# Performance work log

Measured on AMD Instinct MI355X. Metric: run time of the kernel, lower is better.

The kernel has to match this reference:

```python
import jax, jax.numpy as jnp
import numpy as np

B, S, D, O = 8, 2048, 1024, 1024  # batch, seq_len, state_dim(=input_dim), output_dim


def setup_inputs() -> dict:
    key = jax.random.key(0)
    k_in, k_a, k_bc = jax.random.split(key, 3)
    inputs = jax.random.normal(k_in, (B, S, D), dtype=jnp.float32)
    # Stable diagonal transition (|A| < 1) so the 2048-step recurrence stays bounded.
    A = jax.random.uniform(k_a, (D,), minval=-0.99, maxval=0.99, dtype=jnp.float32)
    BC = jax.random.normal(k_bc, (D, O), dtype=jnp.float32) / D
    return {"inputs": inputs, "A": A, "BC": BC}


def reference(inputs, A, BC):
    # Diagonal LTI recurrence: h_t = A * h_{t-1} + x_t ; out_t = h_t @ BC
    # h0 = zeros (the module's h0 Parameter is initialized to zeros).
    x_tfirst = jnp.swapaxes(inputs, 0, 1)  # [S, B, D]

    def step(h, x_t):
        h = h * A + x_t
        return h, h

    h0 = jnp.zeros((inputs.shape[0], A.shape[0]), dtype=inputs.dtype)
    _, hs = jax.lax.scan(step, h0, x_tfirst)  # hs: [S, B, D]
    # Single fused projection over all timesteps instead of per-step matmuls.
    out = jnp.einsum('sbd,do->bso', hs, BC)  # [B, S, O]
    return out
```

## Files before the change

kernel.cpp:

```cpp
#include <hip/hip_runtime.h>
#include <hip/hip_bf16.h>

#define BB 8
#define SS 2048
#define DD 1024
#define OO 1024
#define MM (BB * SS)
#define KK DD
#define NN OO
#define CC 32
#define LL 64

typedef __bf16 bf16x8 __attribute__((ext_vector_type(8)));
typedef __bf16 bf16x4 __attribute__((ext_vector_type(4)));
typedef float floatx4 __attribute__((ext_vector_type(4)));

__global__ __launch_bounds__(256) void scan_carry(const float* __restrict__ x,
                                                  const float* __restrict__ A,
                                                  float* __restrict__ carry) {
    const int i4 = threadIdx.x;
    const int c = blockIdx.x;
    const int b = blockIdx.y;
    const float4 a = ((const float4*)A)[i4];
    const float4* xp = (const float4*)(x + ((size_t)b * SS + (size_t)c * LL) * DD) + i4;
    float4 h = make_float4(0.f, 0.f, 0.f, 0.f);
#pragma unroll 8
    for (int t = 0; t < LL; ++t) {
        const float4 v = xp[(size_t)t * (DD / 4)];
        h.x = fmaf(h.x, a.x, v.x);
        h.y = fmaf(h.y, a.y, v.y);
        h.z = fmaf(h.z, a.z, v.z);
        h.w = fmaf(h.w, a.w, v.w);
    }
    ((float4*)carry)[((size_t)b * CC + c) * (DD / 4) + i4] = h;
}

__global__ void chunk_scan(const float* __restrict__ carry, const float* __restrict__ A,
                           float* __restrict__ Hprev) {
    const int idx = blockIdx.x * 256 + threadIdx.x;
    const int d = idx & (DD - 1);
    const int b = idx >> 10;
    const float a = A[d];
    float aL = a;
#pragma unroll
    for (int i = 0; i < 6; ++i) aL *= aL;
    float h = 0.f;
#pragma unroll
    for (int c = 0; c < CC; ++c) {
        const size_t o = ((size_t)b * CC + c) * DD + d;
        Hprev[o] = h;
        h = fmaf(aL, h, carry[o]);
    }
}

__global__ __launch_bounds__(256) void scan_emit(const float* __restrict__ x,
                                                 const float* __restrict__ A,
                                                 const float* __restrict__ Hprev,
                                                 __bf16* __restrict__ hs) {
    const int i4 = threadIdx.x;
    const int c = blockIdx.x;
    const int b = blockIdx.y;
    const float4 a = ((const float4*)A)[i4];
    float4 h = ((const float4*)Hprev)[((size_t)b * CC + c) * (DD / 4) + i4];
    const size_t base = ((size_t)b * SS + (size_t)c * LL) * DD;
    const float4* xp = (const float4*)(x + base) + i4;
    bf16x4* hp = (bf16x4*)(hs + base) + i4;
#pragma unroll 4
    for (int t = 0; t < LL; ++t) {
        const float4 v = xp[(size_t)t * (DD / 4)];
        h.x = fmaf(h.x, a.x, v.x);
        h.y = fmaf(h.y, a.y, v.y);
        h.z = fmaf(h.z, a.z, v.z);
        h.w = fmaf(h.w, a.w, v.w);
        bf16x4 o;
        o[0] = (__bf16)h.x; o[1] = (__bf16)h.y; o[2] = (__bf16)h.z; o[3] = (__bf16)h.w;
        hp[(size_t)t * (DD / 4)] = o;
    }
}

__global__ void transpose_cast(const float* __restrict__ BC, __bf16* __restrict__ BCt) {
    __shared__ float tile[32][33];
    const int tx = threadIdx.x & 31;
    const int ty = threadIdx.x >> 5;
    const int o0 = blockIdx.x * 32;
    const int d0 = blockIdx.y * 32;
#pragma unroll
    for (int i = 0; i < 4; ++i) {
        const int dd = ty + i * 8;
        tile[dd][tx] = BC[(size_t)(d0 + dd) * OO + o0 + tx];
    }
    __syncthreads();
#pragma unroll
    for (int i = 0; i < 4; ++i) {
        const int oo = ty + i * 8;
        BCt[(size_t)(o0 + oo) * DD + d0 + tx] = (__bf16)tile[tx][oo];
    }
}

#define TM 128
#define TN 128
#define TK 32

__device__ __forceinline__ void async16(void* lds, const void* g) {
    __builtin_amdgcn_global_load_lds(
        (__attribute__((address_space(1))) void*)(void*)g,
        (__attribute__((address_space(3))) void*)lds, 16, 0, 0);
}

__global__ __launch_bounds__(256) void gemm_bt(const __bf16* __restrict__ Am,
                                               const __bf16* __restrict__ Bt,
                                               float* __restrict__ C) {
    __shared__ __align__(16) __bf16 As[TM * TK];
    __shared__ __align__(16) __bf16 Bs[TN * TK];

    const int tid = threadIdx.x;
    const int wave = tid >> 6;
    const int lane = tid & 63;
    const int wm = (wave >> 1) * 64;
    const int wn = (wave & 1) * 64;
    const int lanelo = lane & 15;
    const int quad = lane >> 4;
    const int tile_m = blockIdx.x * TM;
    const int tile_n = blockIdx.y * TN;

    const int cid0 = tid;
    const int cid1 = tid + 256;
    const int r0 = cid0 >> 2, q0 = (cid0 & 3) * 8;
    const int r1 = cid1 >> 2, q1 = (cid1 & 3) * 8;

    floatx4 acc[4][4];
#pragma unroll
    for (int i = 0; i < 4; ++i)
#pragma unroll
        for (int j = 0; j < 4; ++j) acc[i][j] = (floatx4){0.f, 0.f, 0.f, 0.f};

    for (int k0 = 0; k0 < KK; k0 += TK) {
        __syncthreads();
        async16(&As[cid0 * 8], Am + (size_t)(tile_m + r0) * KK + k0 + q0);
        async16(&As[cid1 * 8], Am + (size_t)(tile_m + r1) * KK + k0 + q1);
        async16(&Bs[cid0 * 8], Bt + (size_t)(tile_n + r0) * KK + k0 + q0);
        async16(&Bs[cid1 * 8], Bt + (size_t)(tile_n + r1) * KK + k0 + q1);
        __syncthreads();

        bf16x8 af[4], bf[4];
#pragma unroll
        for (int i = 0; i < 4; ++i)
            af[i] = *(const bf16x8*)(&As[(wm + i * 16 + lanelo) * TK + quad * 8]);
#pragma unroll
        for (int j = 0; j < 4; ++j)
            bf[j] = *(const bf16x8*)(&Bs[(wn + j * 16 + lanelo) * TK + quad * 8]);

#pragma unroll
        for (int i = 0; i < 4; ++i)
#pragma unroll
            for (int j = 0; j < 4; ++j)
                acc[i][j] = __builtin_amdgcn_mfma_f32_16x16x32_bf16(af[i], bf[j], acc[i][j], 0, 0, 0);
    }

#pragma unroll
    for (int i = 0; i < 4; ++i) {
        const int row = tile_m + wm + i * 16 + quad * 4;
#pragma unroll
        for (int r = 0; r < 4; ++r) {
            float* crow = C + (size_t)(row + r) * NN + tile_n + wn + lanelo;
#pragma unroll
            for (int j = 0; j < 4; ++j) crow[j * 16] = acc[i][j][r];
        }
    }
}

extern "C" void kernel_launch(void* const* d_in, const int* in_sizes, int n_in,
                              void* d_out, int out_size, void* d_ws, size_t ws_size,
                              hipStream_t stream) {
    const float* x  = (const float*)d_in[0];
    const float* A  = (const float*)d_in[1];
    const float* BC = (const float*)d_in[2];
    float* out = (float*)d_out;

    char* ws = (char*)d_ws;
    __bf16* hs   = (__bf16*)ws;
    float* carry = (float*)(ws + 33554432);
    float* Hprev = (float*)(ws + 33554432 + 1048576);
    __bf16* BCt  = (__bf16*)(ws + 33554432 + 2097152);

    scan_carry<<<dim3(CC, BB), 256, 0, stream>>>(x, A, carry);
    transpose_cast<<<dim3(OO / 32, DD / 32), 256, 0, stream>>>(BC, BCt);
    chunk_scan<<<dim3(BB * DD / 256), 256, 0, stream>>>(carry, A, Hprev);
    scan_emit<<<dim3(CC, BB), 256, 0, stream>>>(x, A, Hprev, hs);
    gemm_bt<<<dim3(MM / TM, NN / TN), 256, 0, stream>>>(hs, BCt, out);
}
```

Measured before the change: 180.4 us.

## Double scan chunk count, fuse carry scan with BC transpose, batch loads

Raises the number of sequence chunks from 32 to 64 (length 32 each), doubling the blocks in the carry and emit scan kernels so more CUs are busy during these memory-bound phases. The carry scan and the BC transpose-cast are merged into one launch, removing a kernel launch. Loads of x are grouped eight at a time to raise memory-level parallelism, and chunk_scan preloads all carries into registers before the serial pass. The trade-off is a longer serial chunk_scan, more carry and Hprev traffic, and higher register use in chunk_scan.

Result: no change. 179.0 us (-0.8%).

```diff
diff --git a/kernel.cpp b/kernel.cpp
--- a/kernel.cpp
+++ b/kernel.cpp
@@ -8,48 +8,83 @@
 #define MM (BB * SS)
 #define KK DD
 #define NN OO
-#define CC 32
-#define LL 64
+#define CC 64
+#define LL 32
 
 typedef __bf16 bf16x8 __attribute__((ext_vector_type(8)));
 typedef __bf16 bf16x4 __attribute__((ext_vector_type(4)));
 typedef float floatx4 __attribute__((ext_vector_type(4)));
 
-__global__ __launch_bounds__(256) void scan_carry(const float* __restrict__ x,
+__device__ __forceinline__ float4 fma4(float4 h, float4 a, float4 v) {
+    h.x = fmaf(h.x, a.x, v.x);
+    h.y = fmaf(h.y, a.y, v.y);
+    h.z = fmaf(h.z, a.z, v.z);
+    h.w = fmaf(h.w, a.w, v.w);
+    return h;
+}
+
+__global__ __launch_bounds__(256) void prep(const float* __restrict__ x,
+                                            const float* __restrict__ A,
+                                            float* __restrict__ carry,
+                                            const float* __restrict__ BC,
+                                            __bf16* __restrict__ BCt) {
+    __shared__ float tile[32][33];
+    const int id = blockIdx.x;
+    if (id < BB * CC) {
+        const int c = id & (CC - 1);
+        const int b = id >> 6;
+        const int i4 = threadIdx.x;
+        const float4 a = ((const float4*)A)[i4];
+        const float4* xp = (const float4*)(x + ((size_t)b * SS + (size_t)c * LL) * DD) + i4;
+        float4 h = make_float4(0.f, 0.f, 0.f, 0.f);
+#pragma unroll
+        for (int t0 = 0; t0 < LL; t0 += 8) {
+            float4 v[8];
+#pragma unroll
+            for (int u = 0; u < 8; ++u) v[u] = xp[(size_t)(t0 + u) * (DD / 4)];
+#pragma unroll
+            for (int u = 0; u < 8; ++u) h = fma4(h, a, v[u]);
+        }
+        ((float4*)carry)[((size_t)b * CC + c) * (DD / 4) + i4] = h;
+    } else {
+        const int t = id - BB * CC;
+        const int o0 = (t & 31) * 32;
+        const int d0 = (t >> 5) * 32;
+        const int tx = threadIdx.x & 31;
+        const int ty = threadIdx.x >> 5;
+#pragma unroll
+        for (int i = 0; i < 4; ++i) {
+            const int dd = ty + i * 8;
+            tile[dd][tx] = BC[(size_t)(d0 + dd) * OO + o0 + tx];
+        }
+        __syncthreads();
+#pragma unroll
+        for (int i = 0; i < 4; ++i) {
+            const int oo = ty + i * 8;
+            BCt[(size_t)(o0 + oo) * DD + d0 + tx] = (__bf16)tile[tx][oo];
+        }
+    }
+}
+
+__global__ __launch_bounds__(256) void chunk_scan(const float* __restrict__ carry,
                                                   const float* __restrict__ A,
-                                                  float* __restrict__ carry) {
-    const int i4 = threadIdx.x;
-    const int c = blockIdx.x;
-    const int b = blockIdx.y;
-    const float4 a = ((const float4*)A)[i4];
-    const float4* xp = (const float4*)(x + ((size_t)b * SS + (size_t)c * LL) * DD) + i4;
-    float4 h = make_float4(0.f, 0.f, 0.f, 0.f);
-#pragma unroll 8
-    for (int t = 0; t < LL; ++t) {
-        const float4 v = xp[(size_t)t * (DD / 4)];
-        h.x = fmaf(h.x, a.x, v.x);
-        h.y = fmaf(h.y, a.y, v.y);
-        h.z = fmaf(h.z, a.z, v.z);
-        h.w = fmaf(h.w, a.w, v.w);
-    }
-    ((float4*)carry)[((size_t)b * CC + c) * (DD / 4) + i4] = h;
-}
-
-__global__ void chunk_scan(const float* __restrict__ carry, const float* __restrict__ A,
-                           float* __restrict__ Hprev) {
+                                                  float* __restrict__ Hprev) {
     const int idx = blockIdx.x * 256 + threadIdx.x;
     const int d = idx & (DD - 1);
     const int b = idx >> 10;
     const float a = A[d];
     float aL = a;
 #pragma unroll
-    for (int i = 0; i < 6; ++i) aL *= aL;
+    for (int i = 0; i < 5; ++i) aL *= aL;
+    float ca[CC];
+#pragma unroll
+    for (int c = 0; c < CC; ++c)
+        ca[c] = carry[((size_t)b * CC + c) * DD + d];
     float h = 0.f;
 #pragma unroll
     for (int c = 0; c < CC; ++c) {
-        const size_t o = ((size_t)b * CC + c) * DD + d;
-        Hprev[o] = h;
-        h = fmaf(aL, h, carry[o]);
+        Hprev[((size_t)b * CC + c) * DD + d] = h;
+        h = fmaf(aL, h, ca[c]);
     }
 }
 
@@ -57,43 +92,27 @@
                                                  const float* __restrict__ A,
                                                  const float* __restrict__ Hprev,
                                                  __bf16* __restrict__ hs) {
+    const int id = blockIdx.x;
+    const int c = id & (CC - 1);
+    const int b = id >> 6;
     const int i4 = threadIdx.x;
-    const int c = blockIdx.x;
-    const int b = blockIdx.y;
     const float4 a = ((const float4*)A)[i4];
     float4 h = ((const float4*)Hprev)[((size_t)b * CC + c) * (DD / 4) + i4];
     const size_t base = ((size_t)b * SS + (size_t)c * LL) * DD;
     const float4* xp = (const float4*)(x + base) + i4;
     bf16x4* hp = (bf16x4*)(hs + base) + i4;
-#pragma unroll 4
-    for (int t = 0; t < LL; ++t) {
-        const float4 v = xp[(size_t)t * (DD / 4)];
-        h.x = fmaf(h.x, a.x, v.x);
-        h.y = fmaf(h.y, a.y, v.y);
-        h.z = fmaf(h.z, a.z, v.z);
-        h.w = fmaf(h.w, a.w, v.w);
-        bf16x4 o;
-        o[0] = (__bf16)h.x; o[1] = (__bf16)h.y; o[2] = (__bf16)h.z; o[3] = (__bf16)h.w;
-        hp[(size_t)t * (DD / 4)] = o;
-    }
-}
-
-__global__ void transpose_cast(const float* __restrict__ BC, __bf16* __restrict__ BCt) {
-    __shared__ float tile[32][33];
-    const int tx = threadIdx.x & 31;
-    const int ty = threadIdx.x >> 5;
-    const int o0 = blockIdx.x * 32;
-    const int d0 = blockIdx.y * 32;
-#pragma unroll
-    for (int i = 0; i < 4; ++i) {
-        const int dd = ty + i * 8;
-        tile[dd][tx] = BC[(size_t)(d0 + dd) * OO + o0 + tx];
-    }
-    __syncthreads();
-#pragma unroll
-    for (int i = 0; i < 4; ++i) {
-        const int oo = ty + i * 8;
-        BCt[(size_t)(o0 + oo) * DD + d0 + tx] = (__bf16)tile[tx][oo];
+#pragma unroll
+    for (int t0 = 0; t0 < LL; t0 += 8) {
+        float4 v[8];
+#pragma unroll
+        for (int u = 0; u < 8; ++u) v[u] = xp[(size_t)(t0 + u) * (DD / 4)];
+#pragma unroll
+        for (int u = 0; u < 8; ++u) {
+            h = fma4(h, a, v[u]);
+            bf16x4 o;
+            o[0] = (__bf16)h.x; o[1] = (__bf16)h.y; o[2] = (__bf16)h.z; o[3] = (__bf16)h.w;
+            hp[(size_t)(t0 + u) * (DD / 4)] = o;
+        }
     }
 }
 
@@ -180,12 +199,11 @@
     char* ws = (char*)d_ws;
     __bf16* hs   = (__bf16*)ws;
     float* carry = (float*)(ws + 33554432);
-    float* Hprev = (float*)(ws + 33554432 + 1048576);
-    __bf16* BCt  = (__bf16*)(ws + 33554432 + 2097152);
-
-    scan_carry<<<dim3(CC, BB), 256, 0, stream>>>(x, A, carry);
-    transpose_cast<<<dim3(OO / 32, DD / 32), 256, 0, stream>>>(BC, BCt);
+    float* Hprev = (float*)(ws + 33554432 + 2097152);
+    __bf16* BCt  = (__bf16*)(ws + 33554432 + 4194304);
+
+    prep<<<dim3(BB * CC + 1024), 256, 0, stream>>>(x, A, carry, BC, BCt);
     chunk_scan<<<dim3(BB * DD / 256), 256, 0, stream>>>(carry, A, Hprev);
-    scan_emit<<<dim3(CC, BB), 256, 0, stream>>>(x, A, Hprev, hs);
+    scan_emit<<<dim3(BB * CC), 256, 0, stream>>>(x, A, Hprev, hs);
     gemm_bt<<<dim3(MM / TM, NN / TN), 256, 0, stream>>>(hs, BCt, out);
 }
```
